# Performance work log

Hardware: AMD Instinct MI355X
Metric: run time of the kernel (lower is better)

The kernel has to match this reference:

```python
import jax, jax.numpy as jnp
import numpy as np

B = 1
DEPTH = 2
DIM = 256
HEADS = 8
MLP = 1024
NUM_CLASS = 4
PATCHES = 512
N = PATCHES * (NUM_CLASS + 1)  # 2560
HD = DIM // HEADS


def setup_inputs() -> dict:
    key = jax.random.key(0)
    ks = jax.random.split(key, 8)
    s = lambda k, shape: jax.random.normal(k, shape, jnp.float32) * 0.02
    return {
        "x": jax.random.normal(ks[0], (B, N, DIM), jnp.float32),
        "mask": jax.random.randint(ks[1], (B, NUM_CLASS), 0, 2, jnp.int32),
        "ln1_g": jnp.ones((DEPTH, DIM), jnp.float32),
        "ln1_b": jnp.zeros((DEPTH, DIM), jnp.float32),
        "Wqkv": s(ks[2], (DEPTH, DIM, 3 * DIM)),  # qkv_bias=False
        "Wproj": s(ks[3], (DEPTH, DIM, DIM)),
        "bproj": jnp.zeros((DEPTH, DIM), jnp.float32),
        "ln2_g": jnp.ones((DEPTH, DIM), jnp.float32),
        "ln2_b": jnp.zeros((DEPTH, DIM), jnp.float32),
        "W1": s(ks[4], (DEPTH, DIM, MLP)),
        "b1": jnp.zeros((DEPTH, MLP), jnp.float32),
        "W2": s(ks[5], (DEPTH, MLP, DIM)),
        "b2": jnp.zeros((DEPTH, DIM), jnp.float32),
    }


def layer_norm(x, g, b, eps=1e-5):
    mu = jnp.mean(x, axis=-1, keepdims=True)
    var = jnp.var(x, axis=-1, keepdims=True)
    return (x - mu) * jax.lax.rsqrt(var + eps) * g + b


def build_mask(mask):
    # Vectorized equivalent of mask_gen_fusion: block-diagonal per modality,
    # fusion rows attend everything except columns of missing modalities.
    blk = jnp.arange(N) // PATCHES  # [N], values in 0..NUM_CLASS
    base = blk[:, None] == blk[None, :]  # block diagonal (incl. fusion block)
    fusion_row = blk == NUM_CLASS  # [N]
    col_fusion = blk == NUM_CLASS  # [N]
    mod_ok = mask[:, jnp.clip(blk, 0, NUM_CLASS - 1)] == 1  # [B, N]
    allowed = jnp.where(fusion_row[None, :, None],
                        col_fusion[None, None, :] | mod_ok[:, None, :],
                        base[None, :, :])
    return allowed  # [B, N, N] bool


def reference(x, mask, ln1_g, ln1_b, Wqkv, Wproj, bproj, ln2_g, ln2_b, W1, b1, W2, b2):
    allowed = build_mask(mask)  # [B, N, N]
    scale = HD ** -0.5
    attns = []
    for d in range(DEPTH):
        # MaskedResidual(MaskedPreNormDrop(MaskedAttention))
        h = layer_norm(x, ln1_g[d], ln1_b[d])
        qkv = (h @ Wqkv[d]).reshape(B, N, 3, HEADS, HD)
        q, k, v = jnp.transpose(qkv, (2, 0, 3, 1, 4))  # each [B, H, N, HD]
        scores = jnp.einsum('bhnd,bhmd->bhnm', q, k) * scale
        scores = jnp.where(allowed[:, None, :, :], scores, -jnp.inf)
        attn = jax.nn.softmax(scores, axis=-1)  # [B, H, N, N]
        o = jnp.einsum('bhnm,bhmd->bhnd', attn, v)
        o = jnp.transpose(o, (0, 2, 1, 3)).reshape(B, N, DIM)
        o = o @ Wproj[d] + bproj[d]
        x = x + o
        attns.append(attn)
        # Residual(PreNorm(FeedForward)); F.gelu is exact erf gelu
        h2 = layer_norm(x, ln2_g[d], ln2_b[d])
        ff = jax.nn.gelu(h2 @ W1[d] + b1[d], approximate=False) @ W2[d] + b2[d]
        x = x + ff
    return x, jnp.stack(attns)
```

## Files before the change

### kernel.cpp

```cpp
#include <hip/hip_runtime.h>

#define NTOK 2560
#define NN ((long)NTOK*NTOK)

typedef __attribute__((ext_vector_type(8))) short short8;
typedef __attribute__((ext_vector_type(4))) float f32x4;

__device__ __forceinline__ unsigned short f2bf(float f){
  union { float f; unsigned int u; } v; v.f = f;
  unsigned int u = v.u + 0x7fffu + ((v.u >> 16) & 1u);
  return (unsigned short)(u >> 16);
}

__device__ __forceinline__ f32x4 mfma16(short8 a, short8 b, f32x4 c){
  return __builtin_amdgcn_mfma_f32_16x16x32_bf16(a, b, c, 0, 0, 0);
}

__global__ __launch_bounds__(256) void wt_all_k(
    const float* __restrict__ Wqkv, const float* __restrict__ Wproj,
    const float* __restrict__ W1, const float* __restrict__ W2,
    unsigned short* __restrict__ wqkvt, unsigned short* __restrict__ wprojt,
    unsigned short* __restrict__ w1t, unsigned short* __restrict__ w2t)
{
  __shared__ unsigned short T[64][68];
  int j = blockIdx.x;
  int d = j >= 192; j -= d*192;
  const float* src; unsigned short* dst; int K, N, tk, tn;
  if (j < 48){        src = Wqkv  + d*196608; dst = wqkvt  + d*196608; K=256;  N=768;  tk=j/12; tn=j-tk*12; }
  else if (j < 64){   j-=48;  src = Wproj + d*65536;  dst = wprojt + d*65536;  K=256;  N=256;  tk=j>>2; tn=j&3; }
  else if (j < 128){  j-=64;  src = W1    + d*262144; dst = w1t    + d*262144; K=256;  N=1024; tk=j>>4; tn=j&15; }
  else {              j-=128; src = W2    + d*262144; dst = w2t    + d*262144; K=1024; N=256;  tk=j>>2; tn=j&3; }
  int k0 = tk*64, n0 = tn*64;
  int r = threadIdx.x >> 2, c0 = (threadIdx.x & 3) * 16;
  const float* p = src + (long)(k0+r)*N + n0 + c0;
  #pragma unroll
  for (int e4 = 0; e4 < 4; e4++){
    f32x4 v = *(const f32x4*)(p + e4*4);
    #pragma unroll
    for (int e = 0; e < 4; e++) T[r][c0 + e4*4 + e] = f2bf(v[e]);
  }
  __syncthreads();
  unsigned short* q = dst + (long)(n0+r)*K + k0 + c0;
  short8 o0, o1;
  #pragma unroll
  for (int e = 0; e < 8; e++){ o0[e] = (short)T[c0+e][r]; o1[e] = (short)T[c0+8+e][r]; }
  *(short8*)q = o0;
  *(short8*)(q+8) = o1;
}

__device__ __forceinline__ void p_unit_body(
    int u, const unsigned short* __restrict__ qbf, const unsigned short* __restrict__ kbf,
    const float* __restrict__ rinv_ws, float* __restrict__ attn_out,
    const int* __restrict__ mask, char* smem)
{
  float (*P32)[268] = (float (*)[268])smem;
  int tid = threadIdx.x, lane = tid & 63, w = tid >> 6;
  int cb = u % 5, t2 = u / 5, tile = t2 % 80, h = t2 / 80;
  int row0 = tile * 32;
  int rblk = row0 >> 9;
  unsigned bits;
  if (rblk < 4) bits = 1u << rblk;
  else {
    bits = 16u;
    #pragma unroll
    for (int m=0; m<4; m++) if (mask[m]==1) bits |= (1u<<m);
  }
  long base = (long)h*NN + (long)row0*NTOK + cb*512;
  if (!((bits >> cb) & 1)){
    f32x4 z = {0.f,0.f,0.f,0.f};
    #pragma unroll
    for (int i=0;i<16;i++){
      int idx = tid + i*256;
      int rl = idx >> 7, c4 = (idx & 127) << 2;
      *(f32x4*)&attn_out[base + (long)rl*NTOK + c4] = z;
    }
    return;
  }
  int kk = (lane>>4)*8, l15 = lane & 15, rgrp = (lane>>4)*4;
  short8 aq0 = *(const short8*)&qbf[(h*NTOK + row0 + l15)*32 + kk];
  short8 aq1 = *(const short8*)&qbf[(h*NTOK + row0 + 16 + l15)*32 + kk];
  float rinv[8];
  #pragma unroll
  for (int r=0;r<4;r++){
    rinv[r]   = rinv_ws[h*NTOK + row0 + rgrp + r];
    rinv[4+r] = rinv_ws[h*NTOK + row0 + 16 + rgrp + r];
  }
  #pragma unroll
  for (int hf=0; hf<2; hf++){
    #pragma unroll
    for (int ct=0; ct<4; ct++){
      int cl = w*64 + ct*16 + l15;
      short8 bk = *(const short8*)&kbf[(h*NTOK + cb*512 + hf*256 + cl)*32 + kk];
      f32x4 s0 = {}; s0 = mfma16(aq0, bk, s0);
      f32x4 s1 = {}; s1 = mfma16(aq1, bk, s1);
      #pragma unroll
      for (int r=0;r<4;r++){
        P32[rgrp + r][cl]      = __expf(s0[r]) * rinv[r];
        P32[16 + rgrp + r][cl] = __expf(s1[r]) * rinv[4+r];
      }
    }
    __syncthreads();
    long hbase = base + hf*256;
    #pragma unroll
    for (int j=0;j<8;j++){
      int qi = j*256 + tid;
      int rl = qi >> 6, qc = (qi & 63)*4;
      *(f32x4*)&attn_out[hbase + (long)rl*NTOK + qc] = *(const f32x4*)&P32[rl][qc];
    }
    __syncthreads();
  }
}

template<int EPI, bool LN>
__global__ __launch_bounds__(256) void gemm2_k(
    const void* __restrict__ Ap,
    const float* __restrict__ lng, const float* __restrict__ lnb,
    const unsigned short* __restrict__ Bt,
    int N, int K,
    const float* __restrict__ bias,
    const float* __restrict__ xin,
    float* __restrict__ xout,
    unsigned short* __restrict__ obf,
    unsigned short* __restrict__ qbf,
    unsigned short* __restrict__ kbf,
    unsigned short* __restrict__ vtbf,
    int gx, int pbase,
    const unsigned short* __restrict__ p_qbf, const unsigned short* __restrict__ p_kbf,
    const float* __restrict__ p_rinv, float* __restrict__ p_attn,
    const int* __restrict__ maskp)
{
  __shared__ __align__(16) char smem[67584];
  if ((int)blockIdx.x >= gx){
    int u = pbase + ((int)blockIdx.x - gx) * (int)gridDim.y + (int)blockIdx.y;
    p_unit_body(u, p_qbf, p_kbf, p_rinv, p_attn, maskp, smem);
    return;
  }
  unsigned short (*As)[264] = (unsigned short (*)[264])smem;
  unsigned short (*Bs)[264] = (unsigned short (*)[264])(smem + 33792);
  int tid = threadIdx.x, lane = tid & 63, w = tid >> 6;
  int wr = w >> 1, wc = w & 1;
  int m0 = blockIdx.y * 64, n0 = blockIdx.x * 64;
  int row = tid >> 2, q4 = tid & 3;
  int l15 = lane & 15;
  f32x4 acc[2][2] = {};

  for (int k0 = 0; k0 < K; k0 += 256){
    if (LN){
      const float* xrow = (const float*)Ap + (m0+row)*256;
      float s = 0.f, s2 = 0.f;
      #pragma unroll
      for (int j=0;j<8;j++){
        const float* p = xrow + (j*4+q4)*8;
        f32x4 va = *(const f32x4*)p;
        f32x4 vb = *(const f32x4*)(p+4);
        #pragma unroll
        for (int e=0;e<4;e++){ s += va[e]+vb[e]; s2 += va[e]*va[e]+vb[e]*vb[e]; }
      }
      s  += __shfl_xor(s, 1);  s2 += __shfl_xor(s2, 1);
      s  += __shfl_xor(s, 2);  s2 += __shfl_xor(s2, 2);
      float mu = s * (1.f/256.f);
      float inv = rsqrtf(s2*(1.f/256.f) - mu*mu + 1e-5f);
      #pragma unroll
      for (int j=0;j<8;j++){
        int c0 = (j*4+q4)*8;
        const float* p = xrow + c0;
        f32x4 va = *(const f32x4*)p;
        f32x4 vb = *(const f32x4*)(p+4);
        f32x4 ga = *(const f32x4*)&lng[c0], gb = *(const f32x4*)&lng[c0+4];
        f32x4 ba = *(const f32x4*)&lnb[c0], bb = *(const f32x4*)&lnb[c0+4];
        short8 o;
        #pragma unroll
        for (int e=0;e<4;e++){
          o[e]   = (short)f2bf((va[e]-mu)*inv*ga[e] + ba[e]);
          o[4+e] = (short)f2bf((vb[e]-mu)*inv*gb[e] + bb[e]);
        }
        *(short8*)&As[row][c0] = o;
      }
    } else {
      const unsigned short* Arow = (const unsigned short*)Ap + (long)(m0+row)*K + k0;
      #pragma unroll
      for (int j=0;j<8;j++){
        int c0 = (j*4+q4)*8;
        *(short8*)&As[row][c0] = *(const short8*)&Arow[c0];
      }
    }
    {
      const unsigned short* Brow = Bt + (long)(n0+row)*K + k0;
      #pragma unroll
      for (int j=0;j<8;j++){
        int c0 = (j*4+q4)*8;
        *(short8*)&Bs[row][c0] = *(const short8*)&Brow[c0];
      }
    }
    __syncthreads();
    #pragma unroll
    for (int ks=0; ks<8; ks++){
      int kc = ks*32 + (lane>>4)*8;
      short8 a0 = *(const short8*)&As[wr*32 + l15][kc];
      short8 a1 = *(const short8*)&As[wr*32 + 16 + l15][kc];
      short8 b0 = *(const short8*)&Bs[wc*32 + l15][kc];
      short8 b1 = *(const short8*)&Bs[wc*32 + 16 + l15][kc];
      acc[0][0] = mfma16(a0,b0,acc[0][0]);
      acc[0][1] = mfma16(a0,b1,acc[0][1]);
      acc[1][0] = mfma16(a1,b0,acc[1][0]);
      acc[1][1] = mfma16(a1,b1,acc[1][1]);
    }
    if (k0 + 256 < K) __syncthreads();
  }

  #pragma unroll
  for (int rt=0; rt<2; rt++)
  #pragma unroll
  for (int ct=0; ct<2; ct++)
  #pragma unroll
  for (int r=0; r<4; r++){
    int rg = m0 + wr*32 + rt*16 + (lane>>4)*4 + r;
    int cg = n0 + wc*32 + ct*16 + l15;
    float v = acc[rt][ct][r];
    if (EPI == 0){
      int which = cg >> 8, h = (cg >> 5) & 7, hd = cg & 31;
      if (which == 0)      qbf[(h*NTOK + rg)*32 + hd] = f2bf(v * 0.17677669529663687f);
      else if (which == 1) kbf[(h*NTOK + rg)*32 + hd] = f2bf(v);
      else                 vtbf[(h*32 + hd)*NTOK + rg] = f2bf(v);
    } else if (EPI == 1){
      xout[rg*N + cg] = xin[rg*N + cg] + v + bias[cg];
    } else {
      float t = v + bias[cg];
      float ge = 0.5f * t * (1.f + erff(t * 0.70710678118654752f));
      obf[rg*N + cg] = f2bf(ge);
    }
  }
}

__global__ __launch_bounds__(256) void attn_o_k(
    const unsigned short* __restrict__ qbf,
    const unsigned short* __restrict__ kbf,
    const unsigned short* __restrict__ vtbf,
    const int* __restrict__ mask,
    float* __restrict__ rinv_ws,
    unsigned short* __restrict__ obf)
{
  __shared__ __align__(16) float P32[32][268];
  __shared__ float O_red[4][32][32];
  __shared__ float reds[4][32];
  __shared__ float rowinv_s[32];

  int tid = threadIdx.x, lane = tid & 63, w = tid >> 6;
  int row0 = blockIdx.x * 32, h = blockIdx.y;
  int rblk = row0 >> 9;
  unsigned bits;
  if (rblk < 4) bits = 1u << rblk;
  else {
    bits = 16u;
    #pragma unroll
    for (int m=0; m<4; m++) if (mask[m] == 1) bits |= (1u << m);
  }
  int kk = (lane >> 4) * 8;
  int l15 = lane & 15;
  int rgrp = (lane >> 4) * 4;
  short8 aq0 = *(const short8*)&qbf[(h*NTOK + row0 + l15)*32 + kk];
  short8 aq1 = *(const short8*)&qbf[(h*NTOK + row0 + 16 + l15)*32 + kk];

  float s_[8] = {0,0,0,0,0,0,0,0};
  f32x4 oacc[2][2] = {};
  for (int b=0; b<5; b++){
    if (!((bits >> b) & 1)) continue;
    #pragma unroll
    for (int hf=0; hf<2; hf++){
      #pragma unroll
      for (int ct=0; ct<4; ct++){
        int cl = w*64 + ct*16 + l15;
        short8 bk = *(const short8*)&kbf[(h*NTOK + b*512 + hf*256 + cl)*32 + kk];
        f32x4 s0 = {}; s0 = mfma16(aq0, bk, s0);
        f32x4 s1 = {}; s1 = mfma16(aq1, bk, s1);
        #pragma unroll
        for (int r=0;r<4;r++){
          float e0 = __expf(s0[r]), e1 = __expf(s1[r]);
          s_[r] += e0; s_[4+r] += e1;
          P32[rgrp + r][cl] = e0;
          P32[16 + rgrp + r][cl] = e1;
        }
      }
      __syncthreads();
      #pragma unroll
      for (int ks2=0; ks2<2; ks2++){
        int kb = (w*2 + ks2)*32 + kk;
        f32x4 pa0a = *(const f32x4*)&P32[l15][kb],      pa0b = *(const f32x4*)&P32[l15][kb+4];
        f32x4 pa1a = *(const f32x4*)&P32[16 + l15][kb], pa1b = *(const f32x4*)&P32[16 + l15][kb+4];
        short8 pa0, pa1;
        #pragma unroll
        for (int e=0;e<4;e++){
          pa0[e] = (short)f2bf(pa0a[e]); pa0[4+e] = (short)f2bf(pa0b[e]);
          pa1[e] = (short)f2bf(pa1a[e]); pa1[4+e] = (short)f2bf(pa1b[e]);
        }
        #pragma unroll
        for (int hc=0; hc<2; hc++){
          short8 bv = *(const short8*)&vtbf[(h*32 + hc*16 + l15)*NTOK + b*512 + hf*256 + kb];
          oacc[0][hc] = mfma16(pa0, bv, oacc[0][hc]);
          oacc[1][hc] = mfma16(pa1, bv, oacc[1][hc]);
        }
      }
      __syncthreads();
    }
  }
  #pragma unroll
  for (int msk=1; msk<16; msk<<=1)
    #pragma unroll
    for (int i=0;i<8;i++) s_[i] += __shfl_xor(s_[i], msk);
  if (l15 == 0){
    #pragma unroll
    for (int r=0;r<4;r++){ reds[w][rgrp + r] = s_[r]; reds[w][16 + rgrp + r] = s_[4+r]; }
  }
  __syncthreads();
  if (tid < 32){
    float inv = 1.f / (reds[0][tid] + reds[1][tid] + reds[2][tid] + reds[3][tid]);
    rowinv_s[tid] = inv;
    rinv_ws[h*NTOK + row0 + tid] = inv;
  }
  __syncthreads();
  #pragma unroll
  for (int rt=0; rt<2; rt++)
    #pragma unroll
    for (int hc=0; hc<2; hc++)
      #pragma unroll
      for (int r=0; r<4; r++)
        O_red[w][rt*16 + rgrp + r][hc*16 + l15] = oacc[rt][hc][r];
  __syncthreads();
  #pragma unroll
  for (int i2=0; i2<2; i2++){
    int i = tid + i2*256;
    int rl = i >> 4, c2 = (i & 15) * 2;
    float inv = rowinv_s[rl];
    float o0 = (O_red[0][rl][c2]   + O_red[1][rl][c2]   + O_red[2][rl][c2]   + O_red[3][rl][c2]) * inv;
    float o1 = (O_red[0][rl][c2+1] + O_red[1][rl][c2+1] + O_red[2][rl][c2+1] + O_red[3][rl][c2+1]) * inv;
    unsigned int pk = (unsigned int)f2bf(o0) | ((unsigned int)f2bf(o1) << 16);
    *(unsigned int*)&obf[(row0 + rl)*256 + h*32 + c2] = pk;
  }
}

extern "C" void kernel_launch(void* const* d_in, const int* in_sizes, int n_in,
                              void* d_out, int out_size, void* d_ws, size_t ws_size,
                              hipStream_t stream)
{
  const float* x_in  = (const float*)d_in[0];
  const int*   maskp = (const int*)d_in[1];
  const float* ln1g  = (const float*)d_in[2];
  const float* ln1b  = (const float*)d_in[3];
  const float* Wqkv  = (const float*)d_in[4];
  const float* Wproj = (const float*)d_in[5];
  const float* bproj = (const float*)d_in[6];
  const float* ln2g  = (const float*)d_in[7];
  const float* ln2b  = (const float*)d_in[8];
  const float* W1    = (const float*)d_in[9];
  const float* b1    = (const float*)d_in[10];
  const float* W2    = (const float*)d_in[11];
  const float* b2    = (const float*)d_in[12];
  float* out = (float*)d_out;

  char* ws = (char*)d_ws;
  float* x              = (float*)(ws + 0);
  unsigned short* mbf   = (unsigned short*)(ws + 2621440);
  unsigned short* obf   = (unsigned short*)(ws + 7864320);
  unsigned short* qbf   = (unsigned short*)(ws + 9175040);
  unsigned short* kbf   = (unsigned short*)(ws + 10485760);
  unsigned short* vtbf  = (unsigned short*)(ws + 11796480);
  float* rinv           = (float*)(ws + 13107200);
  unsigned short* wqkvt = (unsigned short*)(ws + 13238272);
  unsigned short* wprojt= (unsigned short*)(ws + 14024704);
  unsigned short* w1t   = (unsigned short*)(ws + 14286848);
  unsigned short* w2t   = (unsigned short*)(ws + 15335424);

  wt_all_k<<<384, 256, 0, stream>>>(Wqkv, Wproj, W1, W2, wqkvt, wprojt, w1t, w2t);

  for (int d=0; d<2; d++){
    const float* xsrc = d ? x : x_in;
    float* attn = out + 655360 + (long)d*52428800;
    gemm2_k<0,true><<<dim3(12,40), 256, 0, stream>>>(xsrc, ln1g + d*256, ln1b + d*256,
        wqkvt + d*196608, 768, 256, nullptr, nullptr, nullptr, nullptr, qbf, kbf, vtbf,
        12, 0, nullptr, nullptr, nullptr, nullptr, nullptr);
    attn_o_k<<<dim3(80,8), 256, 0, stream>>>(qbf, kbf, vtbf, maskp, rinv, obf);
    gemm2_k<1,false><<<dim3(24,40), 256, 0, stream>>>(obf, nullptr, nullptr,
        wprojt + d*65536, 256, 256, bproj + d*256, xsrc, x, nullptr, nullptr, nullptr, nullptr,
        4, 0, qbf, kbf, rinv, attn, maskp);
    gemm2_k<2,true><<<dim3(46,40), 256, 0, stream>>>(x, ln2g + d*256, ln2b + d*256,
        w1t + d*262144, 1024, 256, b1 + d*1024, nullptr, nullptr, mbf, nullptr, nullptr, nullptr,
        16, 800, qbf, kbf, rinv, attn, maskp);
    float* xo = d ? out : x;
    gemm2_k<1,false><<<dim3(34,40), 256, 0, stream>>>(mbf, nullptr, nullptr,
        w2t + d*262144, 256, 1024, b2 + d*256, x, xo, nullptr, nullptr, nullptr, nullptr,
        4, 2000, qbf, kbf, rinv, attn, maskp);
  }
}
```

Measured before the change: 186.2 us.

## Split attention-prob units into compute and zero-fill work, rescheduling across kernels

Replaces the uniform 2000-unit per-layer attention-probability tile enumeration with an enumeration of only the tiles the block mask allows (at most 1152). Masked tiles become separate zero-fill units, which are tacked onto the QKV GEMM and the attention-output kernel grids. Compute units are now spread across the proj and the two MLP GEMMs with smaller extra grids. This is meant to stop launching blocks that only zero memory or exit early inside the heavy GEMM launches, and to overlap the zero stores with earlier kernels. It relies on fixed hand-computed unit counts and offsets that must match the mask layout exactly.

```diff
diff --git a/kernel.cpp b/kernel.cpp
--- a/kernel.cpp
+++ b/kernel.cpp
@@ -48,34 +48,46 @@
   *(short8*)(q+8) = o1;
 }
 
+__device__ __forceinline__ void zero_unit_body(int u, const int* __restrict__ mask,
+                                               float* __restrict__ attn_out)
+{
+  int h = u / 320, rem = u - h*320;
+  int tile, cb;
+  if (rem < 256){
+    tile = rem >> 2;
+    int zi = rem & 3, rblk = tile >> 4;
+    cb = zi + (zi >= rblk);
+  } else {
+    int fz = rem - 256;
+    tile = 64 + (fz >> 2);
+    cb = fz & 3;
+    if (mask[cb] == 1) return;
+  }
+  long base = (long)h*NN + (long)tile*32*NTOK + cb*512;
+  f32x4 z = {0.f,0.f,0.f,0.f};
+  int tid = threadIdx.x;
+  #pragma unroll
+  for (int i=0;i<16;i++){
+    int idx = tid + i*256;
+    int rl = idx >> 7, c4 = (idx & 127) << 2;
+    *(f32x4*)&attn_out[base + (long)rl*NTOK + c4] = z;
+  }
+}
+
 __device__ __forceinline__ void p_unit_body(
     int u, const unsigned short* __restrict__ qbf, const unsigned short* __restrict__ kbf,
     const float* __restrict__ rinv_ws, float* __restrict__ attn_out,
     const int* __restrict__ mask, char* smem)
 {
+  if (u >= 1152) return;
+  int h, tile, cb;
+  if (u < 512){ h = u >> 6; tile = u & 63; cb = tile >> 4; }
+  else if (u < 640){ int v = u - 512; h = v >> 4; tile = 64 + (v & 15); cb = 4; }
+  else { int v = u - 640; h = v >> 6; tile = 64 + ((v >> 2) & 15); cb = v & 3; if (mask[cb] != 1) return; }
   float (*P32)[268] = (float (*)[268])smem;
   int tid = threadIdx.x, lane = tid & 63, w = tid >> 6;
-  int cb = u % 5, t2 = u / 5, tile = t2 % 80, h = t2 / 80;
   int row0 = tile * 32;
-  int rblk = row0 >> 9;
-  unsigned bits;
-  if (rblk < 4) bits = 1u << rblk;
-  else {
-    bits = 16u;
-    #pragma unroll
-    for (int m=0; m<4; m++) if (mask[m]==1) bits |= (1u<<m);
-  }
   long base = (long)h*NN + (long)row0*NTOK + cb*512;
-  if (!((bits >> cb) & 1)){
-    f32x4 z = {0.f,0.f,0.f,0.f};
-    #pragma unroll
-    for (int i=0;i<16;i++){
-      int idx = tid + i*256;
-      int rl = idx >> 7, c4 = (idx & 127) << 2;
-      *(f32x4*)&attn_out[base + (long)rl*NTOK + c4] = z;
-    }
-    return;
-  }
   int kk = (lane>>4)*8, l15 = lane & 15, rgrp = (lane>>4)*4;
   short8 aq0 = *(const short8*)&qbf[(h*NTOK + row0 + l15)*32 + kk];
   short8 aq1 = *(const short8*)&qbf[(h*NTOK + row0 + 16 + l15)*32 + kk];
@@ -111,7 +123,7 @@
   }
 }
 
-template<int EPI, bool LN>
+template<int EPI, bool LN, int CG>
 __global__ __launch_bounds__(256) void gemm2_k(
     const void* __restrict__ Ap,
     const float* __restrict__ lng, const float* __restrict__ lnb,
@@ -124,15 +136,16 @@
     unsigned short* __restrict__ qbf,
     unsigned short* __restrict__ kbf,
     unsigned short* __restrict__ vtbf,
-    int gx, int pbase,
+    int gx, int zbase,
     const unsigned short* __restrict__ p_qbf, const unsigned short* __restrict__ p_kbf,
     const float* __restrict__ p_rinv, float* __restrict__ p_attn,
     const int* __restrict__ maskp)
 {
   __shared__ __align__(16) char smem[67584];
   if ((int)blockIdx.x >= gx){
-    int u = pbase + ((int)blockIdx.x - gx) * (int)gridDim.y + (int)blockIdx.y;
-    p_unit_body(u, p_qbf, p_kbf, p_rinv, p_attn, maskp, smem);
+    int u = zbase + ((int)blockIdx.x - gx) * (int)gridDim.y + (int)blockIdx.y;
+    if (CG == 1) zero_unit_body(u, maskp, p_attn);
+    else if (CG == 2) p_unit_body(u, p_qbf, p_kbf, p_rinv, p_attn, maskp, smem);
     return;
   }
   unsigned short (*As)[264] = (unsigned short (*)[264])smem;
@@ -238,12 +251,19 @@
     const unsigned short* __restrict__ vtbf,
     const int* __restrict__ mask,
     float* __restrict__ rinv_ws,
-    unsigned short* __restrict__ obf)
+    unsigned short* __restrict__ obf,
+    int zbase, float* __restrict__ p_attn)
 {
   __shared__ __align__(16) float P32[32][268];
   __shared__ float O_red[4][32][32];
   __shared__ float reds[4][32];
   __shared__ float rowinv_s[32];
+
+  if ((int)blockIdx.x >= 80){
+    int u = zbase + ((int)blockIdx.x - 80) * (int)gridDim.y + (int)blockIdx.y;
+    zero_unit_body(u, mask, p_attn);
+    return;
+  }
 
   int tid = threadIdx.x, lane = tid & 63, w = tid >> 6;
   int row0 = blockIdx.x * 32, h = blockIdx.y;
@@ -375,19 +395,19 @@
   for (int d=0; d<2; d++){
     const float* xsrc = d ? x : x_in;
     float* attn = out + 655360 + (long)d*52428800;
-    gemm2_k<0,true><<<dim3(12,40), 256, 0, stream>>>(xsrc, ln1g + d*256, ln1b + d*256,
+    gemm2_k<0,true,1><<<dim3(38,40), 256, 0, stream>>>(xsrc, ln1g + d*256, ln1b + d*256,
         wqkvt + d*196608, 768, 256, nullptr, nullptr, nullptr, nullptr, qbf, kbf, vtbf,
-        12, 0, nullptr, nullptr, nullptr, nullptr, nullptr);
-    attn_o_k<<<dim3(80,8), 256, 0, stream>>>(qbf, kbf, vtbf, maskp, rinv, obf);
-    gemm2_k<1,false><<<dim3(24,40), 256, 0, stream>>>(obf, nullptr, nullptr,
+        12, 0, nullptr, nullptr, nullptr, attn, maskp);
+    attn_o_k<<<dim3(270,8), 256, 0, stream>>>(qbf, kbf, vtbf, maskp, rinv, obf, 1040, attn);
+    gemm2_k<1,false,2><<<dim3(14,40), 256, 0, stream>>>(obf, nullptr, nullptr,
         wprojt + d*65536, 256, 256, bproj + d*256, xsrc, x, nullptr, nullptr, nullptr, nullptr,
         4, 0, qbf, kbf, rinv, attn, maskp);
-    gemm2_k<2,true><<<dim3(46,40), 256, 0, stream>>>(x, ln2g + d*256, ln2b + d*256,
+    gemm2_k<2,true,2><<<dim3(26,40), 256, 0, stream>>>(x, ln2g + d*256, ln2b + d*256,
         w1t + d*262144, 1024, 256, b1 + d*1024, nullptr, nullptr, mbf, nullptr, nullptr, nullptr,
-        16, 800, qbf, kbf, rinv, attn, maskp);
+        16, 400, qbf, kbf, rinv, attn, maskp);
     float* xo = d ? out : x;
-    gemm2_k<1,false><<<dim3(34,40), 256, 0, stream>>>(mbf, nullptr, nullptr,
+    gemm2_k<1,false,2><<<dim3(13,40), 256, 0, stream>>>(mbf, nullptr, nullptr,
         w2t + d*262144, 256, 1024, b2 + d*256, x, xo, nullptr, nullptr, nullptr, nullptr,
-        4, 2000, qbf, kbf, rinv, attn, maskp);
-  }
-}
+        4, 800, qbf, kbf, rinv, attn, maskp);
+  }
+}
```

Result: slower. 196.1 us (+5.3%).
